# Kernel tuning notes

Hardware: AMD Instinct MI355X
Metric: run time of the kernel (lower is better)

Reference implementation:

```python
import jax, jax.numpy as jnp
import numpy as np

# NAM: in_features independent 1->H->H->1 MLPs (FeatureNNs), batched over the
# feature dimension F instead of a Python loop of tiny kernels.
# inputs: (B, F); W1,b1: (F, H); W2: (F, H, H); b2: (F, H); W3: (F, H); b3: (F,)

def setup_inputs() -> dict:
    key = jax.random.key(0)
    ks = jax.random.split(key, 7)
    B, F, H = 8192, 128, 64
    s1 = 1.0  # fan_in = 1 for first layer
    s2 = 1.0 / np.sqrt(H)
    return {
        "inputs": jax.random.normal(ks[0], (B, F), dtype=jnp.float32),
        "W1": jax.random.normal(ks[1], (F, H), dtype=jnp.float32) * s1,
        "b1": jax.random.normal(ks[2], (F, H), dtype=jnp.float32) * 0.01,
        "W2": jax.random.normal(ks[3], (F, H, H), dtype=jnp.float32) * s2,
        "b2": jax.random.normal(ks[4], (F, H), dtype=jnp.float32) * 0.01,
        "W3": jax.random.normal(ks[5], (F, H), dtype=jnp.float32) * s2,
        "b3": jax.random.normal(ks[6], (F,), dtype=jnp.float32) * 0.01,
    }


def reference(inputs, W1, b1, W2, b2, W3, b3):
    # Layer 1: scalar input per feature -> hidden.  (B,F,1)*(F,H) -> (B,F,H)
    h1 = jax.nn.relu(inputs[:, :, None] * W1[None, :, :] + b1[None, :, :])
    # Layer 2: per-feature hidden->hidden batched matmul.
    h2 = jax.nn.relu(jnp.einsum("bfh,fhk->bfk", h1, W2) + b2[None, :, :])
    # Output layer: hidden -> scalar per feature.
    fnn = jnp.einsum("bfh,fh->bf", h2, W3) + b3[None, :]  # (B, F)
    out = fnn.sum(axis=-1)  # (B,)  additive model output
    return (out, fnn)
```

## Files before the change

kernel.cpp:

```cpp
#include <hip/hip_runtime.h>

#define B 8192
#define F 128
#define H 64

typedef __attribute__((ext_vector_type(8))) short bf16x8;
typedef __attribute__((ext_vector_type(4))) float f32x4;

static __device__ __forceinline__ unsigned short f32_to_bf16(float v) {
    unsigned int u = __float_as_uint(v);
    unsigned int r = (u + 0x7FFFu + ((u >> 16) & 1u)) >> 16;
    return (unsigned short)r;
}
static __device__ __forceinline__ float bf16_to_f32(unsigned short h) {
    return __uint_as_float(((unsigned int)h) << 16);
}

__global__ __launch_bounds__(256, 3) void nam_main(
    const float* __restrict__ inputs, const float* __restrict__ W1,
    const float* __restrict__ b1, const float* __restrict__ W2,
    const float* __restrict__ b2, const float* __restrict__ W3,
    const float* __restrict__ b3, float* __restrict__ fnn_out)
{
    const int tid = threadIdx.x;
    const int f = blockIdx.y;
    const int b0 = blockIdx.x * 256;

    const float* W1f = W1 + f * H;
    const float* b1f = b1 + f * H;
    const float* W2f = W2 + (size_t)f * H * H;
    const float* b2f = b2 + f * H;
    const float* W3f = W3 + f * H;

    __shared__ short bhi_s[512 * 8];
    __shared__ short blo_s[512 * 8];

#pragma unroll
    for (int t = tid; t < 512; t += 256) {
        const int n = t & 63;
        const int g = t >> 6;
        const int nt = n >> 4, c = n & 15;
        const int ks = g >> 2, q = g & 3;
        const int slot = (nt * 2 + ks) * 64 + c + 16 * q;
        bf16x8 hv, lv;
#pragma unroll
        for (int jj = 0; jj < 8; ++jj) {
            const float wv = W2f[(g * 8 + jj) * H + n];
            const unsigned short hi = f32_to_bf16(wv);
            const unsigned short lo = f32_to_bf16(wv - bf16_to_f32(hi));
            hv[jj] = (short)hi;
            lv[jj] = (short)lo;
        }
        *(bf16x8*)&bhi_s[slot * 8] = hv;
        *(bf16x8*)&blo_s[slot * 8] = lv;
    }

    const int lane = tid & 63;
    const int w    = tid >> 6;
    const int q    = lane >> 4;
    const int col  = lane & 15;

    float w1v[16], b1v[16];
#pragma unroll
    for (int ks = 0; ks < 2; ++ks)
#pragma unroll
        for (int j = 0; j < 8; ++j) {
            w1v[ks * 8 + j] = W1f[ks * 32 + q * 8 + j];
            b1v[ks * 8 + j] = b1f[ks * 32 + q * 8 + j];
        }
    float b2v[4], w3v[4];
#pragma unroll
    for (int nt = 0; nt < 4; ++nt) {
        b2v[nt] = b2f[nt * 16 + col];
        w3v[nt] = W3f[nt * 16 + col];
    }
    const float b3f = b3[f];

    __syncthreads();

    bf16x8 bhi[4][2], blo[4][2];
#pragma unroll
    for (int nt = 0; nt < 4; ++nt)
#pragma unroll
        for (int ks = 0; ks < 2; ++ks) {
            const int slot = (nt * 2 + ks) * 64 + lane;
            bhi[nt][ks] = *(bf16x8*)&bhi_s[slot * 8];
            blo[nt][ks] = *(bf16x8*)&blo_s[slot * 8];
        }

#pragma unroll 1
    for (int mt = 0; mt < 4; ++mt) {
        const int rbase = b0 + w * 64 + mt * 16;
        const float x = inputs[(size_t)(rbase + col) * F + f];

        f32x4 acc[4];
#pragma unroll
        for (int nt = 0; nt < 4; ++nt) {
            acc[nt][0] = b2v[nt]; acc[nt][1] = b2v[nt];
            acc[nt][2] = b2v[nt]; acc[nt][3] = b2v[nt];
        }

#pragma unroll
        for (int ks = 0; ks < 2; ++ks) {
            bf16x8 ahi, alo;
#pragma unroll
            for (int j = 0; j < 8; ++j) {
                float h1 = fmaxf(fmaf(x, w1v[ks * 8 + j], b1v[ks * 8 + j]), 0.0f);
                const unsigned short hi = f32_to_bf16(h1);
                const unsigned short lo = f32_to_bf16(h1 - bf16_to_f32(hi));
                ahi[j] = (short)hi;
                alo[j] = (short)lo;
            }
#pragma unroll
            for (int nt = 0; nt < 4; ++nt) {
                acc[nt] = __builtin_amdgcn_mfma_f32_16x16x32_bf16(ahi, bhi[nt][ks], acc[nt], 0, 0, 0);
                acc[nt] = __builtin_amdgcn_mfma_f32_16x16x32_bf16(ahi, blo[nt][ks], acc[nt], 0, 0, 0);
                acc[nt] = __builtin_amdgcn_mfma_f32_16x16x32_bf16(alo, bhi[nt][ks], acc[nt], 0, 0, 0);
            }
        }

        float s[4];
#pragma unroll
        for (int reg = 0; reg < 4; ++reg) {
            float t = 0.0f;
#pragma unroll
            for (int nt = 0; nt < 4; ++nt)
                t = fmaf(fmaxf(acc[nt][reg], 0.0f), w3v[nt], t);
            s[reg] = t;
        }
#pragma unroll
        for (int m_ = 1; m_ <= 8; m_ <<= 1)
#pragma unroll
            for (int reg = 0; reg < 4; ++reg)
                s[reg] += __shfl_xor(s[reg], m_, 64);
        if (col == 0) {
#pragma unroll
            for (int reg = 0; reg < 4; ++reg)
                fnn_out[(size_t)(rbase + 4 * q + reg) * F + f] = s[reg] + b3f;
        }
    }
}

__global__ __launch_bounds__(256) void nam_reduce(
    const float* __restrict__ fnn, float* __restrict__ out)
{
    const int tid = threadIdx.x;
    const int r = tid >> 5;
    const int c = tid & 31;
    const int b = blockIdx.x * 8 + r;

    const float4* row = (const float4*)(fnn + (size_t)b * F);
    float4 v = row[c];
    float s = v.x + v.y + v.z + v.w;
#pragma unroll
    for (int off = 16; off > 0; off >>= 1)
        s += __shfl_down(s, off, 32);
    if (c == 0) out[b] = s;
}

extern "C" void kernel_launch(void* const* d_in, const int* in_sizes, int n_in,
                              void* d_out, int out_size, void* d_ws, size_t ws_size,
                              hipStream_t stream) {
    const float* inputs = (const float*)d_in[0];
    const float* W1     = (const float*)d_in[1];
    const float* b1     = (const float*)d_in[2];
    const float* W2     = (const float*)d_in[3];
    const float* b2     = (const float*)d_in[4];
    const float* W3     = (const float*)d_in[5];
    const float* b3     = (const float*)d_in[6];

    float* out = (float*)d_out;
    float* fnn = out + B;

    nam_main<<<dim3(B / 256, F), 256, 0, stream>>>(inputs, W1, b1, W2, b2, W3,
                                                   b3, fnn);
    nam_reduce<<<dim3(B / 8), 256, 0, stream>>>(fnn, out);
}
```

Baseline: 112.8 us.

## Fuse row reduction via atomics, prefetch inputs, truncate activation split with perm

Removes the separate reduction kernel by having each block atomically add its per-feature outputs into the final row sums, with a memset to zero them first. It also hoists the four input loads before the barrier so they overlap the W2 staging. The activation hi/lo bf16 split now uses truncation plus byte-permute packing instead of round-to-nearest conversions. The risks are atomic contention on each output row (128 features per row), non-deterministic summation order, and slightly different rounding in the hi/lo split.

```diff
diff --git a/kernel.cpp b/kernel.cpp
--- a/kernel.cpp
+++ b/kernel.cpp
@@ -7,7 +7,7 @@
 typedef __attribute__((ext_vector_type(8))) short bf16x8;
 typedef __attribute__((ext_vector_type(4))) float f32x4;
 
-static __device__ __forceinline__ unsigned short f32_to_bf16(float v) {
+static __device__ __forceinline__ unsigned short f32_to_bf16_rne(float v) {
     unsigned int u = __float_as_uint(v);
     unsigned int r = (u + 0x7FFFu + ((u >> 16) & 1u)) >> 16;
     return (unsigned short)r;
@@ -20,7 +20,8 @@
     const float* __restrict__ inputs, const float* __restrict__ W1,
     const float* __restrict__ b1, const float* __restrict__ W2,
     const float* __restrict__ b2, const float* __restrict__ W3,
-    const float* __restrict__ b3, float* __restrict__ fnn_out)
+    const float* __restrict__ b3, float* __restrict__ out,
+    float* __restrict__ fnn_out)
 {
     const int tid = threadIdx.x;
     const int f = blockIdx.y;
@@ -46,8 +47,8 @@
 #pragma unroll
         for (int jj = 0; jj < 8; ++jj) {
             const float wv = W2f[(g * 8 + jj) * H + n];
-            const unsigned short hi = f32_to_bf16(wv);
-            const unsigned short lo = f32_to_bf16(wv - bf16_to_f32(hi));
+            const unsigned short hi = f32_to_bf16_rne(wv);
+            const unsigned short lo = f32_to_bf16_rne(wv - bf16_to_f32(hi));
             hv[jj] = (short)hi;
             lv[jj] = (short)lo;
         }
@@ -76,6 +77,11 @@
     }
     const float b3f = b3[f];
 
+    float x4[4];
+#pragma unroll
+    for (int mt = 0; mt < 4; ++mt)
+        x4[mt] = inputs[(size_t)(b0 + w * 64 + mt * 16 + col) * F + f];
+
     __syncthreads();
 
     bf16x8 bhi[4][2], blo[4][2];
@@ -91,7 +97,7 @@
 #pragma unroll 1
     for (int mt = 0; mt < 4; ++mt) {
         const int rbase = b0 + w * 64 + mt * 16;
-        const float x = inputs[(size_t)(rbase + col) * F + f];
+        const float x = x4[mt];
 
         f32x4 acc[4];
 #pragma unroll
@@ -102,20 +108,24 @@
 
 #pragma unroll
         for (int ks = 0; ks < 2; ++ks) {
-            bf16x8 ahi, alo;
+            union { unsigned int u[4]; bf16x8 v; } Ah, Al;
 #pragma unroll
-            for (int j = 0; j < 8; ++j) {
-                float h1 = fmaxf(fmaf(x, w1v[ks * 8 + j], b1v[ks * 8 + j]), 0.0f);
-                const unsigned short hi = f32_to_bf16(h1);
-                const unsigned short lo = f32_to_bf16(h1 - bf16_to_f32(hi));
-                ahi[j] = (short)hi;
-                alo[j] = (short)lo;
+            for (int t = 0; t < 4; ++t) {
+                const float r0 = fmaxf(fmaf(x, w1v[ks * 8 + 2 * t],     b1v[ks * 8 + 2 * t]),     0.0f);
+                const float r1 = fmaxf(fmaf(x, w1v[ks * 8 + 2 * t + 1], b1v[ks * 8 + 2 * t + 1]), 0.0f);
+                const unsigned int u0 = __float_as_uint(r0);
+                const unsigned int u1 = __float_as_uint(r1);
+                const float l0 = r0 - __uint_as_float(u0 & 0xFFFF0000u);
+                const float l1 = r1 - __uint_as_float(u1 & 0xFFFF0000u);
+                Ah.u[t] = __builtin_amdgcn_perm(u1, u0, 0x07060302);
+                Al.u[t] = __builtin_amdgcn_perm(__float_as_uint(l1),
+                                                __float_as_uint(l0), 0x07060302);
             }
 #pragma unroll
             for (int nt = 0; nt < 4; ++nt) {
-                acc[nt] = __builtin_amdgcn_mfma_f32_16x16x32_bf16(ahi, bhi[nt][ks], acc[nt], 0, 0, 0);
-                acc[nt] = __builtin_amdgcn_mfma_f32_16x16x32_bf16(ahi, blo[nt][ks], acc[nt], 0, 0, 0);
-                acc[nt] = __builtin_amdgcn_mfma_f32_16x16x32_bf16(alo, bhi[nt][ks], acc[nt], 0, 0, 0);
+                acc[nt] = __builtin_amdgcn_mfma_f32_16x16x32_bf16(Ah.v, bhi[nt][ks], acc[nt], 0, 0, 0);
+                acc[nt] = __builtin_amdgcn_mfma_f32_16x16x32_bf16(Ah.v, blo[nt][ks], acc[nt], 0, 0, 0);
+                acc[nt] = __builtin_amdgcn_mfma_f32_16x16x32_bf16(Al.v, bhi[nt][ks], acc[nt], 0, 0, 0);
             }
         }
 
@@ -135,27 +145,14 @@
                 s[reg] += __shfl_xor(s[reg], m_, 64);
         if (col == 0) {
 #pragma unroll
-            for (int reg = 0; reg < 4; ++reg)
-                fnn_out[(size_t)(rbase + 4 * q + reg) * F + f] = s[reg] + b3f;
+            for (int reg = 0; reg < 4; ++reg) {
+                const int row = rbase + 4 * q + reg;
+                const float val = s[reg] + b3f;
+                fnn_out[(size_t)row * F + f] = val;
+                atomicAdd(&out[row], val);
+            }
         }
     }
-}
-
-__global__ __launch_bounds__(256) void nam_reduce(
-    const float* __restrict__ fnn, float* __restrict__ out)
-{
-    const int tid = threadIdx.x;
-    const int r = tid >> 5;
-    const int c = tid & 31;
-    const int b = blockIdx.x * 8 + r;
-
-    const float4* row = (const float4*)(fnn + (size_t)b * F);
-    float4 v = row[c];
-    float s = v.x + v.y + v.z + v.w;
-#pragma unroll
-    for (int off = 16; off > 0; off >>= 1)
-        s += __shfl_down(s, off, 32);
-    if (c == 0) out[b] = s;
 }
 
 extern "C" void kernel_launch(void* const* d_in, const int* in_sizes, int n_in,
@@ -172,7 +169,7 @@
     float* out = (float*)d_out;
     float* fnn = out + B;
 
+    hipMemsetAsync(out, 0, B * sizeof(float), stream);
     nam_main<<<dim3(B / 256, F), 256, 0, stream>>>(inputs, W1, b1, W2, b2, W3,
-                                                   b3, fnn);
-    nam_reduce<<<dim3(B / 8), 256, 0, stream>>>(fnn, out);
+                                                   b3, out, fnn);
 }
```

After: 107.7 us. 1.05x faster.
